# Optimization experiments

Hardware: AMD Instinct MI355X
Metric: run time of the kernel (lower is better)

## Reference

```python
import jax, jax.numpy as jnp
import numpy as np
from jax import lax

WINDOW_SIZE = 11
SIGMA = 1.5
IMG_RANGE = 2.0
MS_WEIGHTS = np.array([0.0448, 0.2856, 0.3001, 0.2363, 0.1333], dtype=np.float32)


def _gauss_window(k=WINDOW_SIZE, sigma=SIGMA):
    x = np.arange(k, dtype=np.float64) - k // 2
    g = np.exp(-(x ** 2) / (2.0 * sigma ** 2))
    g = g / g.sum()
    return jnp.asarray(np.outer(g, g), dtype=jnp.float32)  # [k, k]


def _dwconv(x, win):
    # depthwise valid conv, groups = channels (torch conv2d weight [C,1,k,k])
    c = x.shape[1]
    k = win.shape[0]
    rhs = jnp.broadcast_to(win[None, None], (c, 1, k, k))
    return lax.conv_general_dilated(
        x, rhs, window_strides=(1, 1), padding='VALID',
        dimension_numbers=('NCHW', 'OIHW', 'NCHW'), feature_group_count=c)


def _ssim(img1, img2, win, img_range):
    mu1 = _dwconv(img1, win)
    mu2 = _dwconv(img2, win)
    mu1_sq, mu2_sq, mu1_mu2 = mu1 * mu1, mu2 * mu2, mu1 * mu2
    sigma1_sq = _dwconv(img1 * img1, win) - mu1_sq
    sigma2_sq = _dwconv(img2 * img2, win) - mu2_sq
    sigma12 = _dwconv(img1 * img2, win) - mu1_mu2
    C1 = (0.01 * img_range) ** 2
    C2 = (0.03 * img_range) ** 2
    v1 = 2.0 * sigma12 + C2
    v2 = sigma1_sq + sigma2_sq + C2
    cs = jnp.mean(v1 / v2)
    ssim_map = (2.0 * mu1_mu2 + C1) * v1 / ((mu1_sq + mu2_sq + C1) * v2)
    return jnp.mean(ssim_map), cs


def _avg_pool2(x):
    b, c, h, w = x.shape
    return x.reshape(b, c, h // 2, 2, w // 2, 2).mean(axis=(3, 5))


def _msssim_loss(img1, img2):
    win = _gauss_window()
    weights = jnp.asarray(MS_WEIGHTS)
    sims = []
    mcs = None
    for _ in range(len(MS_WEIGHTS)):  # fixed 5 pyramid levels
        sim, mcs = _ssim(img1, img2, win, IMG_RANGE)
        sims.append(sim)
        img1 = _avg_pool2(img1)
        img2 = _avg_pool2(img2)
    ssims = jnp.stack(sims)
    # faithful to source: cs from LAST level powered by weights[-1]
    output = mcs ** weights[-1] * jnp.prod(ssims ** weights)
    return 1.0 - output


def setup_inputs() -> dict:
    key = jax.random.key(0)
    k1, k2 = jax.random.split(key)
    img1 = jax.random.normal(k1, (16, 3, 512, 512), dtype=jnp.float32)
    # correlated pair so per-level SSIM/CS means stay positive (fractional powers)
    img2 = img1 + 0.05 * jax.random.normal(k2, (16, 3, 512, 512), dtype=jnp.float32)
    return {'img1': img1, 'img2': img2}


def reference(img1, img2):
    return _msssim_loss(img1, img2)
```

## Files before the change

### kernel.cpp

```cpp
#include <hip/hip_runtime.h>
#include <cmath>

typedef float vf2 __attribute__((ext_vector_type(2)));

struct G11 { float v[11]; };

#define NB0 12288
#define NB1 3072
#define NB2 768
#define NB3 192
#define NB4 48
#define NPART 16368

struct Smem {
    float4 sAB2[21][43];
    float4 vrt[16][45];
    float red[8];
};

template<int J>
__device__ __forceinline__ void vtap(vf2 m, const float (&g)[11], vf2 (&amu)[4], vf2 (&aq)[4]) {
    vf2 t = m * m;
    vf2 q = { t.x + t.y, m.x * m.y };
#pragma unroll
    for (int i = 0; i < 4; ++i) {
        if (J - i >= 0 && J - i <= 10) {
            vf2 gs = { g[J - i], g[J - i] };
            amu[i] = __builtin_elementwise_fma(gs, m, amu[i]);
            aq[i]  = __builtin_elementwise_fma(gs, q, aq[i]);
        }
    }
}

template<int T>
__device__ __forceinline__ void htap(const float4 V, const float (&g)[11], vf2 (&amu)[4], vf2 (&aq)[4]) {
    vf2 mt = { V.x, V.y }, qt = { V.z, V.w };
#pragma unroll
    for (int i = 0; i < 4; ++i) {
        if (T - i >= 0 && T - i <= 10) {
            vf2 gs = { g[T - i], g[T - i] };
            amu[i] = __builtin_elementwise_fma(gs, mt, amu[i]);
            aq[i]  = __builtin_elementwise_fma(gs, qt, aq[i]);
        }
    }
}

struct PyrOut {
    float *a1, *b1, *a2, *b2, *a3, *b3, *a4, *b4;
};

template<int L>
__device__ __forceinline__ void ssim_body(Smem& sm, int tbx, int tby, int z,
    const float* __restrict__ i1, const float* __restrict__ i2,
    const G11 gw, float2* __restrict__ partials, int pidx, const PyrOut* po)
{
    constexpr int Hl = 512 >> L;
    constexpr int Hv = Hl - 10;
    const int tid = threadIdx.x;
    const int bx = tbx * 32, by = tby * 32;

    float g[11];
#pragma unroll
    for (int j = 0; j < 11; ++j) g[j] = gw.v[j];

    {
        const float* p1 = i1 + (size_t)z * Hl * Hl;
        const float* p2 = i2 + (size_t)z * Hl * Hl;
        for (int i = tid; i < 441; i += 256) {
            int rp = i / 21, cp = i - rp * 21, c = 2 * cp;
            int y = by + 2 * rp, x = bx + c;
            float2 a0 = {0.f,0.f}, a1 = a0, b0 = a0, b1 = a0;
            if (y < Hl && x < Hl) {
                const float* r1p = p1 + (size_t)y * Hl + x;
                a0 = *(const float2*)r1p;
                a1 = *(const float2*)(r1p + Hl);
                const float* r2p = p2 + (size_t)y * Hl + x;
                b0 = *(const float2*)r2p;
                b1 = *(const float2*)(r2p + Hl);
            }
            sm.sAB2[rp][c]     = make_float4(a0.x, b0.x, a1.x, b1.x);
            sm.sAB2[rp][c + 1] = make_float4(a0.y, b0.y, a1.y, b1.y);
        }
    }
    __syncthreads();

    if constexpr (L == 0) {
        float2* pp = (float2*)&sm.vrt[0][0];
        {
            int py = tid >> 4, px = tid & 15;
            float4 q0 = sm.sAB2[py][2 * px];
            float4 q1 = sm.sAB2[py][2 * px + 1];
            float l1a = 0.25f * ((q0.x + q1.x) + (q0.z + q1.z));
            float l1b = 0.25f * ((q0.y + q1.y) + (q0.w + q1.w));
            size_t o = (size_t)z * 65536 + (size_t)(tby * 16 + py) * 256 + (tbx * 16 + px);
            po->a1[o] = l1a; po->b1[o] = l1b;
            pp[tid] = make_float2(l1a, l1b);
        }
        __syncthreads();
        if (tid < 64) {
            int y = tid >> 3, x = tid & 7;
            float2 p00 = pp[(2*y)*16 + 2*x],     p01 = pp[(2*y)*16 + 2*x + 1];
            float2 p10 = pp[(2*y+1)*16 + 2*x],   p11 = pp[(2*y+1)*16 + 2*x + 1];
            float l2a = 0.25f * ((p00.x + p01.x) + (p10.x + p11.x));
            float l2b = 0.25f * ((p00.y + p01.y) + (p10.y + p11.y));
            size_t o2 = (size_t)z * 16384 + (size_t)(tby * 8 + y) * 128 + (tbx * 8 + x);
            po->a2[o2] = l2a; po->b2[o2] = l2b;

            int b3 = (16 * (tid >> 2) + 2 * (tid & 3)) & 63;
            float a00 = __shfl(l2a, b3),     a01 = __shfl(l2a, b3 + 1);
            float a10 = __shfl(l2a, b3 + 8), a11 = __shfl(l2a, b3 + 9);
            float c00 = __shfl(l2b, b3),     c01 = __shfl(l2b, b3 + 1);
            float c10 = __shfl(l2b, b3 + 8), c11 = __shfl(l2b, b3 + 9);
            float l3a = 0.25f * ((a00 + a01) + (a10 + a11));
            float l3b = 0.25f * ((c00 + c01) + (c10 + c11));
            if (tid < 16) {
                size_t o3 = (size_t)z * 4096 + (size_t)(tby * 4 + (tid >> 2)) * 64 + (tbx * 4 + (tid & 3));
                po->a3[o3] = l3a; po->b3[o3] = l3b;
            }
            int b4 = (8 * (tid >> 1) + 2 * (tid & 1)) & 63;
            float d00 = __shfl(l3a, b4),     d01 = __shfl(l3a, b4 + 1);
            float d10 = __shfl(l3a, b4 + 4), d11 = __shfl(l3a, b4 + 5);
            float e00 = __shfl(l3b, b4),     e01 = __shfl(l3b, b4 + 1);
            float e10 = __shfl(l3b, b4 + 4), e11 = __shfl(l3b, b4 + 5);
            float l4a = 0.25f * ((d00 + d01) + (d10 + d11));
            float l4b = 0.25f * ((e00 + e01) + (e10 + e11));
            if (tid < 4) {
                size_t o4 = (size_t)z * 1024 + (size_t)(tby * 2 + (tid >> 1)) * 32 + (tbx * 2 + (tid & 1));
                po->a4[o4] = l4a; po->b4[o4] = l4b;
            }
        }
        __syncthreads();
    }

    float ssim_l = 0.f, cs_l = 0.f;

#pragma unroll
    for (int p = 0; p < 2; ++p) {
        if (p) __syncthreads();

        if (tid < 168) {
            int c = tid % 42, ch = tid / 42;
            int rp0 = 8 * p + 2 * ch;
            vf2 amu[4], aq[4];
#pragma unroll
            for (int i = 0; i < 4; ++i) { amu[i] = (vf2){0.f,0.f}; aq[i] = (vf2){0.f,0.f}; }
#define VPAIR(K) { float4 Q = sm.sAB2[rp0 + (K)][c];                  \
                   vtap<2*(K)>((vf2){Q.x, Q.y}, g, amu, aq);          \
                   vtap<2*(K)+1>((vf2){Q.z, Q.w}, g, amu, aq); }
            VPAIR(0) VPAIR(1) VPAIR(2) VPAIR(3) VPAIR(4) VPAIR(5) VPAIR(6)
#undef VPAIR
            int r0 = 4 * ch;
#pragma unroll
            for (int i = 0; i < 4; ++i)
                sm.vrt[r0 + i][c] = make_float4(amu[i].x, amu[i].y, aq[i].x, aq[i].y);
        }
        __syncthreads();

        if (tid < 128) {
            int row = tid >> 3, oct = tid & 7, c0 = 4 * oct;
            int oy = by + 16 * p + row;
            vf2 amu[4], aq[4];
#pragma unroll
            for (int i = 0; i < 4; ++i) { amu[i] = (vf2){0.f,0.f}; aq[i] = (vf2){0.f,0.f}; }
#define HT(T) htap<(T)>(sm.vrt[row][c0 + (T)], g, amu, aq);
            HT(0) HT(1) HT(2) HT(3) HT(4) HT(5) HT(6)
            HT(7) HT(8) HT(9) HT(10) HT(11) HT(12) HT(13)
#undef HT
            if (oy < Hv) {
#pragma unroll
                for (int i = 0; i < 4; ++i) {
                    int ox = bx + c0 + i;
                    if (ox < Hv) {
                        vf2 mu = amu[i], qq = aq[i];
                        float ab = mu.x * mu.y;
                        vf2 t = mu * mu;
                        float aabb = t.x + t.y;
                        float n1 = fmaf(2.f, ab, 0.0004f);
                        float d1 = aabb + 0.0004f;
                        float v1 = fmaf(2.f, qq.y - ab, 0.0036f);
                        float v2 = (qq.x - aabb) + 0.0036f;
                        float rden = __builtin_amdgcn_rcpf(d1 * v2);
                        cs_l   = fmaf(v1 * d1, rden, cs_l);
                        ssim_l = fmaf(n1 * v1, rden, ssim_l);
                    }
                }
            }
        }
    }

#pragma unroll
    for (int off = 32; off > 0; off >>= 1) {
        ssim_l += __shfl_down(ssim_l, off);
        cs_l   += __shfl_down(cs_l, off);
    }
    int wave = tid >> 6, lane = tid & 63;
    if (lane == 0) { sm.red[wave] = ssim_l; sm.red[4 + wave] = cs_l; }
    __syncthreads();
    if (tid == 0) {
        float ss = sm.red[0] + sm.red[1] + sm.red[2] + sm.red[3];
        float cc = sm.red[4] + sm.red[5] + sm.red[6] + sm.red[7];
        partials[pidx] = make_float2(ss, cc);
    }
}

__global__ __launch_bounds__(256, 6) void ssim_l0_kernel(
    const float* __restrict__ img1, const float* __restrict__ img2,
    const G11 gw, float2* __restrict__ partials, const PyrOut po)
{
    __shared__ Smem sm;
    int pidx = ((int)blockIdx.z * 16 + (int)blockIdx.y) * 16 + (int)blockIdx.x;
    ssim_body<0>(sm, blockIdx.x, blockIdx.y, blockIdx.z, img1, img2, gw, partials, pidx, &po);
}

__global__ __launch_bounds__(256, 6) void ssim_rest_kernel(
    const G11 gw, float2* __restrict__ partials, const PyrOut po)
{
    __shared__ Smem sm;
    int b = blockIdx.x;
    if (b < 3072) {
        int lb = b;        int z = lb >> 6; int r = lb & 63; int tby = r >> 3; int tbx = r & 7;
        ssim_body<1>(sm, tbx, tby, z, po.a1, po.b1, gw, partials, 12288 + lb, nullptr);
    } else if (b < 3840) {
        int lb = b - 3072; int z = lb >> 4; int r = lb & 15; int tby = r >> 2; int tbx = r & 3;
        ssim_body<2>(sm, tbx, tby, z, po.a2, po.b2, gw, partials, 15360 + lb, nullptr);
    } else if (b < 4032) {
        int lb = b - 3840; int z = lb >> 2; int r = lb & 3;  int tby = r >> 1; int tbx = r & 1;
        ssim_body<3>(sm, tbx, tby, z, po.a3, po.b3, gw, partials, 16128 + lb, nullptr);
    } else {
        int lb = b - 4032;
        ssim_body<4>(sm, 0, 0, lb, po.a4, po.b4, gw, partials, 16320 + lb, nullptr);
    }
}

__global__ __launch_bounds__(1024) void msssim_reduce_kernel(
    const float2* __restrict__ partials, float* __restrict__ out)
{
    __shared__ double sred[16][2];
    __shared__ double lev[10];
    const int NB[5]  = {NB0, NB1, NB2, NB3, NB4};
    const int OFF[5] = {0, NB0, NB0 + NB1, NB0 + NB1 + NB2, NB0 + NB1 + NB2 + NB3};
    const int tid = threadIdx.x;
    const int wv = tid >> 6, ln = tid & 63;

    for (int l = 0; l < 5; ++l) {
        double s = 0.0, c = 0.0;
        for (int i = tid; i < NB[l]; i += 1024) {
            float2 p = partials[OFF[l] + i];
            s += (double)p.x; c += (double)p.y;
        }
#pragma unroll
        for (int off = 32; off > 0; off >>= 1) {
            s += __shfl_down(s, off);
            c += __shfl_down(c, off);
        }
        if (ln == 0) { sred[wv][0] = s; sred[wv][1] = c; }
        __syncthreads();
        if (tid == 0) {
            double ss = 0.0, cc = 0.0;
            for (int w = 0; w < 16; ++w) { ss += sred[w][0]; cc += sred[w][1]; }
            lev[l] = ss; lev[5 + l] = cc;
        }
        __syncthreads();
    }

    if (tid == 0) {
        const double counts[5] = {
            48.0 * 502.0 * 502.0,
            48.0 * 246.0 * 246.0,
            48.0 * 118.0 * 118.0,
            48.0 * 54.0 * 54.0,
            48.0 * 22.0 * 22.0
        };
        const double w[5] = { (double)0.0448f, (double)0.2856f, (double)0.3001f,
                              (double)0.2363f, (double)0.1333f };
        double prod = 1.0;
        for (int i = 0; i < 5; ++i) prod *= pow(lev[i] / counts[i], w[i]);
        double mcs = lev[9] / counts[4];
        double output = pow(mcs, w[4]) * prod;
        out[0] = (float)(1.0 - output);
    }
}

extern "C" void kernel_launch(void* const* d_in, const int* in_sizes, int n_in,
                              void* d_out, int out_size, void* d_ws, size_t ws_size,
                              hipStream_t stream) {
    const float* img1 = (const float*)d_in[0];
    const float* img2 = (const float*)d_in[1];
    float* out = (float*)d_out;

    G11 gw;
    {
        double w[11]; double s = 0.0;
        for (int i = 0; i < 11; ++i) { double x = (double)(i - 5); w[i] = std::exp(-(x * x) / 4.5); s += w[i]; }
        for (int i = 0; i < 11; ++i) gw.v[i] = (float)(w[i] / s);
    }

    char* ws = (char*)d_ws;
    float2* partials = (float2*)ws;
    float* base = (float*)(ws + 131072);
    PyrOut po;
    size_t o = 0;
    po.a1 = base + o; o += (size_t)48 * 65536;
    po.b1 = base + o; o += (size_t)48 * 65536;
    po.a2 = base + o; o += (size_t)48 * 16384;
    po.b2 = base + o; o += (size_t)48 * 16384;
    po.a3 = base + o; o += (size_t)48 * 4096;
    po.b3 = base + o; o += (size_t)48 * 4096;
    po.a4 = base + o; o += (size_t)48 * 1024;
    po.b4 = base + o; o += (size_t)48 * 1024;

    ssim_l0_kernel<<<dim3(16, 16, 48), dim3(256), 0, stream>>>(
        img1, img2, gw, partials, po);

    ssim_rest_kernel<<<dim3(4080), dim3(256), 0, stream>>>(gw, partials, po);

    msssim_reduce_kernel<<<dim3(1), dim3(1024), 0, stream>>>(partials, out);
}
```

Measured before the change: 197.5 us.

## Fuse final reduction into last block of rest kernel via atomic counter

Removes the separate single-block reduce kernel launch by having the last finishing block of the pyramid-level kernel, detected through an atomic counter reset in the level-0 kernel, perform the final MS-SSIM reduction with 256 threads. It also preloads the shared-memory operands for the vertical and horizontal tap passes into register arrays before the FMA chains. The aim is to save one launch plus its gap and to batch LDS reads, at the cost of a threadfence and atomic per block, more register pressure, and a reduce done by fewer threads.

```diff
diff --git a/kernel.cpp b/kernel.cpp
--- a/kernel.cpp
+++ b/kernel.cpp
@@ -11,11 +11,13 @@
 #define NB3 192
 #define NB4 48
 #define NPART 16368
+#define NREST 4080
 
 struct Smem {
     float4 sAB2[21][43];
     float4 vrt[16][45];
     float red[8];
+    int isLast;
 };
 
 template<int J>
@@ -141,12 +143,14 @@
         if (tid < 168) {
             int c = tid % 42, ch = tid / 42;
             int rp0 = 8 * p + 2 * ch;
+            float4 Q[7];
+#pragma unroll
+            for (int k = 0; k < 7; ++k) Q[k] = sm.sAB2[rp0 + k][c];
             vf2 amu[4], aq[4];
 #pragma unroll
             for (int i = 0; i < 4; ++i) { amu[i] = (vf2){0.f,0.f}; aq[i] = (vf2){0.f,0.f}; }
-#define VPAIR(K) { float4 Q = sm.sAB2[rp0 + (K)][c];                  \
-                   vtap<2*(K)>((vf2){Q.x, Q.y}, g, amu, aq);          \
-                   vtap<2*(K)+1>((vf2){Q.z, Q.w}, g, amu, aq); }
+#define VPAIR(K) { vtap<2*(K)>((vf2){Q[K].x, Q[K].y}, g, amu, aq);    \
+                   vtap<2*(K)+1>((vf2){Q[K].z, Q[K].w}, g, amu, aq); }
             VPAIR(0) VPAIR(1) VPAIR(2) VPAIR(3) VPAIR(4) VPAIR(5) VPAIR(6)
 #undef VPAIR
             int r0 = 4 * ch;
@@ -159,10 +163,13 @@
         if (tid < 128) {
             int row = tid >> 3, oct = tid & 7, c0 = 4 * oct;
             int oy = by + 16 * p + row;
+            float4 V[14];
+#pragma unroll
+            for (int t = 0; t < 14; ++t) V[t] = sm.vrt[row][c0 + t];
             vf2 amu[4], aq[4];
 #pragma unroll
             for (int i = 0; i < 4; ++i) { amu[i] = (vf2){0.f,0.f}; aq[i] = (vf2){0.f,0.f}; }
-#define HT(T) htap<(T)>(sm.vrt[row][c0 + (T)], g, amu, aq);
+#define HT(T) htap<(T)>(V[T], g, amu, aq);
             HT(0) HT(1) HT(2) HT(3) HT(4) HT(5) HT(6)
             HT(7) HT(8) HT(9) HT(10) HT(11) HT(12) HT(13)
 #undef HT
@@ -205,15 +212,19 @@
 
 __global__ __launch_bounds__(256, 6) void ssim_l0_kernel(
     const float* __restrict__ img1, const float* __restrict__ img2,
-    const G11 gw, float2* __restrict__ partials, const PyrOut po)
+    const G11 gw, float2* __restrict__ partials, int* __restrict__ counter,
+    const PyrOut po)
 {
     __shared__ Smem sm;
+    if (blockIdx.x == 0 && blockIdx.y == 0 && blockIdx.z == 0 && threadIdx.x == 0)
+        *counter = 0;
     int pidx = ((int)blockIdx.z * 16 + (int)blockIdx.y) * 16 + (int)blockIdx.x;
     ssim_body<0>(sm, blockIdx.x, blockIdx.y, blockIdx.z, img1, img2, gw, partials, pidx, &po);
 }
 
 __global__ __launch_bounds__(256, 6) void ssim_rest_kernel(
-    const G11 gw, float2* __restrict__ partials, const PyrOut po)
+    const G11 gw, float2* __restrict__ partials, int* __restrict__ counter,
+    float* __restrict__ out, const PyrOut po)
 {
     __shared__ Smem sm;
     int b = blockIdx.x;
@@ -230,21 +241,26 @@
         int lb = b - 4032;
         ssim_body<4>(sm, 0, 0, lb, po.a4, po.b4, gw, partials, 16320 + lb, nullptr);
     }
-}
-
-__global__ __launch_bounds__(1024) void msssim_reduce_kernel(
-    const float2* __restrict__ partials, float* __restrict__ out)
-{
-    __shared__ double sred[16][2];
-    __shared__ double lev[10];
+
+    const int tid = threadIdx.x;
+    __threadfence();
+    if (tid == 0) {
+        int prev = atomicAdd(counter, 1);
+        sm.isLast = (prev == NREST - 1);
+    }
+    __syncthreads();
+    if (!sm.isLast) return;
+    __threadfence();
+
+    double* lev = (double*)&sm.vrt[0][0];
+    double* sred = lev + 16;
     const int NB[5]  = {NB0, NB1, NB2, NB3, NB4};
     const int OFF[5] = {0, NB0, NB0 + NB1, NB0 + NB1 + NB2, NB0 + NB1 + NB2 + NB3};
-    const int tid = threadIdx.x;
     const int wv = tid >> 6, ln = tid & 63;
 
     for (int l = 0; l < 5; ++l) {
         double s = 0.0, c = 0.0;
-        for (int i = tid; i < NB[l]; i += 1024) {
+        for (int i = tid; i < NB[l]; i += 256) {
             float2 p = partials[OFF[l] + i];
             s += (double)p.x; c += (double)p.y;
         }
@@ -253,11 +269,11 @@
             s += __shfl_down(s, off);
             c += __shfl_down(c, off);
         }
-        if (ln == 0) { sred[wv][0] = s; sred[wv][1] = c; }
+        if (ln == 0) { sred[wv * 2] = s; sred[wv * 2 + 1] = c; }
         __syncthreads();
         if (tid == 0) {
             double ss = 0.0, cc = 0.0;
-            for (int w = 0; w < 16; ++w) { ss += sred[w][0]; cc += sred[w][1]; }
+            for (int w = 0; w < 4; ++w) { ss += sred[w * 2]; cc += sred[w * 2 + 1]; }
             lev[l] = ss; lev[5 + l] = cc;
         }
         __syncthreads();
@@ -297,7 +313,8 @@
 
     char* ws = (char*)d_ws;
     float2* partials = (float2*)ws;
-    float* base = (float*)(ws + 131072);
+    int* counter = (int*)(ws + 131072);
+    float* base = (float*)(ws + 131072 + 256);
     PyrOut po;
     size_t o = 0;
     po.a1 = base + o; o += (size_t)48 * 65536;
@@ -310,9 +327,8 @@
     po.b4 = base + o; o += (size_t)48 * 1024;
 
     ssim_l0_kernel<<<dim3(16, 16, 48), dim3(256), 0, stream>>>(
-        img1, img2, gw, partials, po);
-
-    ssim_rest_kernel<<<dim3(4080), dim3(256), 0, stream>>>(gw, partials, po);
-
-    msssim_reduce_kernel<<<dim3(1), dim3(1024), 0, stream>>>(partials, out);
-}
+        img1, img2, gw, partials, counter, po);
+
+    ssim_rest_kernel<<<dim3(NREST), dim3(256), 0, stream>>>(
+        gw, partials, counter, out, po);
+}
```

After: 442.6 us. 2.24x slower.
